# Performance work log

Measured on AMD Instinct MI355X. Metric: run time of the kernel, lower is better.

The kernel has to match this reference:

```python
import jax, jax.numpy as jnp
import numpy as np

B, N, K, C = 4, 4096, 16, 128
BN_EPS = 1e-5


def setup_inputs() -> dict:
    key = jax.random.key(0)
    ks = jax.random.split(key, 16)
    def f(i, shape, s=0.05):
        return jax.random.normal(ks[i], shape, dtype=jnp.float32) * s
    return dict(
        pose_enc=f(0, (B, N, K, 4), 1.0),
        knn_idx=jax.random.randint(ks[1], (B, N, K), 0, N),
        new_points=f(2, (B, N, C), 1.0),
        wq=f(3, (C, C)), wk=f(4, (C, C)), wv=f(5, (C, C)),
        g_w1=f(6, (C, C)), g_b1=jnp.zeros((C,), jnp.float32),
        g_w2=f(7, (C, C)), g_b2=jnp.zeros((C,), jnp.float32),
        d_w1=f(8, (C, 4)), d_b1=jnp.zeros((C,), jnp.float32),
        d_w2=f(9, (C, C)), d_b2=jnp.zeros((C,), jnp.float32),
        c1_w=f(10, (C, C)), c1_b=jnp.zeros((C,), jnp.float32),
        bn1_g=jnp.ones((C,), jnp.float32), bn1_b=jnp.zeros((C,), jnp.float32),
        c2_w=f(11, (C, C)), c2_b=jnp.zeros((C,), jnp.float32),
        bn2_g=jnp.ones((C,), jnp.float32), bn2_b=jnp.zeros((C,), jnp.float32),
    )


def _bn(x, g, b):
    # BatchNorm1d in training mode: stats over (B, N) per channel, biased var
    m = jnp.mean(x, axis=(0, 1))
    v = jnp.mean(jnp.square(x - m), axis=(0, 1))
    return (x - m) * jax.lax.rsqrt(v + BN_EPS) * g + b


def reference(pose_enc, knn_idx, new_points, wq, wk, wv,
              g_w1, g_b1, g_w2, g_b2, d_w1, d_b1, d_w2, d_b2,
              c1_w, c1_b, bn1_g, bn1_b, c2_w, c2_b, bn2_g, bn2_b):
    # fc_delta: (B,N,K,4) -> (B,N,K,C)
    pos = jax.nn.relu(pose_enc @ d_w1.T + d_b1) @ d_w2.T + d_b2
    # CONV2 (1x1 conv == per-point linear) + BN + ReLU on new_points
    x = jax.nn.relu(_bn(new_points @ c2_w.T + c2_b, bn2_g, bn2_b))  # (B,N,C)
    q = x @ wq.T                                   # (B,N,C)
    kf = x @ wk.T
    vf = x @ wv.T
    gather = jax.vmap(lambda pts, idx: pts[idx])   # (B,N,C),(B,N,K)->(B,N,K,C)
    kk = gather(kf, knn_idx)
    vv = gather(vf, knn_idx)
    # fc_gamma vector attention scores
    h = q[:, :, None, :] - kk + pos                # (B,N,K,C)
    attn = jax.nn.relu(h @ g_w1.T + g_b1) @ g_w2.T + g_b2
    # NOTE: original divides by sqrt(k.size(-1)) where k is the key tensor -> sqrt(C)
    attn = jax.nn.softmax(attn / jnp.sqrt(jnp.float32(C)), axis=-2)
    res = jnp.einsum('bmnf,bmnf->bmf', attn, vv + pos)  # (B,N,C)
    res = jax.nn.relu(_bn(res @ c1_w.T + c1_b, bn1_g, bn1_b)) + new_points
    return res
```

## Files before the change

kernel.cpp:

```cpp
#include <hip/hip_runtime.h>
#include <hip/hip_bf16.h>

typedef __bf16 bf16;
typedef __bf16 bf16x4 __attribute__((ext_vector_type(4)));
typedef __bf16 bf16x8 __attribute__((ext_vector_type(8)));
typedef float  f32x4  __attribute__((ext_vector_type(4)));

#define NN 4096
#define KK 16
#define CC 128
#define BN_TOT 16384

__global__ __launch_bounds__(256) void k_lin(
    const float* __restrict__ A, const float* __restrict__ W,
    const float* __restrict__ bias, float* __restrict__ Y,
    float* __restrict__ partial) {
  __shared__ __attribute__((aligned(16))) bf16 WF[32 * 64 * 8];
  __shared__ __attribute__((aligned(16))) float SF[4][16][132];
  __shared__ float P1[128], P2[128];
  int tid = threadIdx.x, w = tid >> 6, l = tid & 63, quad = l >> 4, col = l & 15;
  int r0 = blockIdx.x * 64;
  int arow = r0 + w * 16 + col;

  if (tid < 128) { P1[tid] = 0.f; P2[tid] = 0.f; }

  for (int e = tid; e < 128 * 16; e += 256) {
    int r = e >> 4, c8 = e & 15;
    const float* p = W + r * CC + c8 * 8;
    f32x4 v0 = *(const f32x4*)p, v1 = *(const f32x4*)(p + 4);
    bf16x8 o;
    for (int i = 0; i < 4; i++) { o[i] = (bf16)v0[i]; o[i + 4] = (bf16)v1[i]; }
    int chunk = (r >> 4) * 4 + (c8 >> 2);
    int lane  = (c8 & 3) * 16 + (r & 15);
    *(bf16x8*)(&WF[(chunk * 64 + lane) * 8]) = o;
  }

  bf16x8 a[4];
  for (int kc = 0; kc < 4; kc++) {
    int c0 = kc * 32 + quad * 8;
    f32x4 y0 = *(const f32x4*)(A + arow * CC + c0);
    f32x4 y1 = *(const f32x4*)(A + arow * CC + c0 + 4);
    bf16x8 o;
    for (int i = 0; i < 4; i++) { o[i] = (bf16)y0[i]; o[i + 4] = (bf16)y1[i]; }
    a[kc] = o;
  }

  f32x4 D[8];
  for (int jb = 0; jb < 8; jb++) {
    float bv = bias[jb * 16 + col];
    D[jb] = (f32x4){bv, bv, bv, bv};
  }
  __syncthreads();
  for (int jb = 0; jb < 8; jb++)
    for (int kc = 0; kc < 4; kc++) {
      bf16x8 bfrag = *(const bf16x8*)(&WF[((jb * 4 + kc) * 64 + l) * 8]);
      D[jb] = __builtin_amdgcn_mfma_f32_16x16x32_bf16(a[kc], bfrag, D[jb], 0, 0, 0);
    }

  for (int jb = 0; jb < 8; jb++) {
    float t1 = D[jb][0] + D[jb][1] + D[jb][2] + D[jb][3];
    float t2 = D[jb][0] * D[jb][0] + D[jb][1] * D[jb][1]
             + D[jb][2] * D[jb][2] + D[jb][3] * D[jb][3];
    t1 += __shfl_xor(t1, 16); t1 += __shfl_xor(t1, 32);
    t2 += __shfl_xor(t2, 16); t2 += __shfl_xor(t2, 32);
    if (quad == 0) {
      atomicAdd(&P1[jb * 16 + col], t1);
      atomicAdd(&P2[jb * 16 + col], t2);
    }
  }

  for (int jb = 0; jb < 8; jb++)
    for (int g = 0; g < 4; g++)
      SF[w][quad * 4 + g][jb * 16 + col] = D[jb][g];
  int orow = r0 + w * 16 + (l >> 2), oc0 = (l & 3) * 32;
  for (int c4 = 0; c4 < 8; c4++) {
    f32x4 v = *(const f32x4*)(&SF[w][l >> 2][oc0 + c4 * 4]);
    *(f32x4*)(Y + orow * CC + oc0 + c4 * 4) = v;
  }

  __syncthreads();
  if (tid < 128) {
    partial[blockIdx.x * 256 + tid] = P1[tid];
    partial[blockIdx.x * 256 + 128 + tid] = P2[tid];
  }
}

__global__ __launch_bounds__(1024) void k_finalize(
    const float* __restrict__ partial, const float* __restrict__ g,
    const float* __restrict__ b, float* __restrict__ stats, int NB) {
  __shared__ float sh[2][1024];
  int t = threadIdx.x, c = t & 127, h = t >> 7;
  float s1 = 0.f, s2 = 0.f;
  for (int blk = h; blk < NB; blk += 8) {
    s1 += partial[blk * 256 + c];
    s2 += partial[blk * 256 + 128 + c];
  }
  sh[0][t] = s1; sh[1][t] = s2;
  __syncthreads();
  if (t < 128) {
    s1 = 0.f; s2 = 0.f;
    for (int hh = 0; hh < 8; hh++) {
      s1 += sh[0][hh * 128 + t];
      s2 += sh[1][hh * 128 + t];
    }
    float mean = s1 * (1.0f / BN_TOT);
    float var  = s2 * (1.0f / BN_TOT) - mean * mean;
    float r = rsqrtf(var + 1e-5f);
    float sc = g[t] * r;
    stats[t] = sc;
    stats[128 + t] = b[t] - mean * sc;
  }
}

__global__ __launch_bounds__(256) void k_qkv(
    const float* __restrict__ Y, const float* __restrict__ stats,
    const float* __restrict__ Wq, const float* __restrict__ Wk, const float* __restrict__ Wv,
    bf16* __restrict__ Qo, bf16* __restrict__ Ko, bf16* __restrict__ Vo) {
  __shared__ __attribute__((aligned(16))) bf16 WF[32 * 64 * 8];
  __shared__ __attribute__((aligned(16))) bf16 S[4][16][132];
  int tid = threadIdx.x, w = tid >> 6, l = tid & 63, quad = l >> 4, col = l & 15;
  int j8 = blockIdx.x >> 3, x8 = blockIdx.x & 7;
  int m = j8 >> 5;
  int rb = x8 * 32 + (j8 & 31);
  int r0 = rb * 64;
  int arow = r0 + w * 16 + col;
  const float* Wg = (m == 0) ? Wq : (m == 1) ? Wk : Wv;
  bf16* Os = (m == 0) ? Qo : (m == 1) ? Ko : Vo;

  for (int e = tid; e < 128 * 16; e += 256) {
    int r = e >> 4, c8 = e & 15;
    const float* p = Wg + r * CC + c8 * 8;
    f32x4 v0 = *(const f32x4*)p, v1 = *(const f32x4*)(p + 4);
    bf16x8 o;
    for (int i = 0; i < 4; i++) { o[i] = (bf16)v0[i]; o[i + 4] = (bf16)v1[i]; }
    int chunk = (r >> 4) * 4 + (c8 >> 2);
    int lane  = (c8 & 3) * 16 + (r & 15);
    *(bf16x8*)(&WF[(chunk * 64 + lane) * 8]) = o;
  }

  bf16x8 a[4];
  for (int kc = 0; kc < 4; kc++) {
    int c0 = kc * 32 + quad * 8;
    f32x4 y0  = *(const f32x4*)(Y + arow * CC + c0);
    f32x4 y1  = *(const f32x4*)(Y + arow * CC + c0 + 4);
    f32x4 sc0 = *(const f32x4*)(stats + c0);
    f32x4 sc1 = *(const f32x4*)(stats + c0 + 4);
    f32x4 sf0 = *(const f32x4*)(stats + 128 + c0);
    f32x4 sf1 = *(const f32x4*)(stats + 128 + c0 + 4);
    bf16x8 o;
    for (int i = 0; i < 4; i++) {
      o[i]     = (bf16)fmaxf(y0[i] * sc0[i] + sf0[i], 0.f);
      o[i + 4] = (bf16)fmaxf(y1[i] * sc1[i] + sf1[i], 0.f);
    }
    a[kc] = o;
  }

  __syncthreads();
  f32x4 D[8];
  for (int jb = 0; jb < 8; jb++) D[jb] = (f32x4){0.f, 0.f, 0.f, 0.f};
  for (int jb = 0; jb < 8; jb++)
    for (int kc = 0; kc < 4; kc++) {
      bf16x8 bfrag = *(const bf16x8*)(&WF[((jb * 4 + kc) * 64 + l) * 8]);
      D[jb] = __builtin_amdgcn_mfma_f32_16x16x32_bf16(a[kc], bfrag, D[jb], 0, 0, 0);
    }
  for (int jb = 0; jb < 8; jb++)
    for (int g = 0; g < 4; g++)
      S[w][quad * 4 + g][jb * 16 + col] = (bf16)D[jb][g];
  int orow = r0 + w * 16 + (l >> 2), oc0 = (l & 3) * 32;
  for (int c8 = 0; c8 < 4; c8++) {
    bf16x8 v = *(const bf16x8*)(&S[w][l >> 2][oc0 + c8 * 8]);
    *(bf16x8*)(Os + orow * CC + oc0 + c8 * 8) = v;
  }
}

__global__ __launch_bounds__(256, 1) void k_attn(
    const bf16* __restrict__ Q, const bf16* __restrict__ Kf, const bf16* __restrict__ Vf,
    const int* __restrict__ knn, const float* __restrict__ pose,
    const float* __restrict__ d_w1, const float* __restrict__ d_b1,
    const float* __restrict__ d_w2, const float* __restrict__ d_b2,
    const float* __restrict__ g_w1, const float* __restrict__ g_b1,
    const float* __restrict__ g_w2, const float* __restrict__ g_b2,
    float* __restrict__ Rs) {
  __shared__ __attribute__((aligned(16))) bf16 WF[96 * 64 * 8];
  __shared__ __attribute__((aligned(16))) bf16 S[4][16][132];
  __shared__ __attribute__((aligned(16))) f32x4 DW1v[128];
  __shared__ float DB1[128];

  int tid = threadIdx.x, w = tid >> 6, l = tid & 63, quad = l >> 4, col = l & 15;
  int bid = (blockIdx.x & 7) * 64 + (blockIdx.x >> 3);

  const float* Wg3[3] = {d_w2, g_w1, g_w2};
  for (int m = 0; m < 3; m++) {
    const float* Wg = Wg3[m];
    for (int e = tid; e < 128 * 16; e += 256) {
      int r = e >> 4, c8 = e & 15;
      const float* p = Wg + r * CC + c8 * 8;
      f32x4 v0 = *(const f32x4*)p, v1 = *(const f32x4*)(p + 4);
      bf16x8 o;
      for (int i = 0; i < 4; i++) { o[i] = (bf16)v0[i]; o[i + 4] = (bf16)v1[i]; }
      int chunk = m * 32 + (r >> 4) * 4 + (c8 >> 2);
      int lane  = (c8 & 3) * 16 + (r & 15);
      *(bf16x8*)(&WF[(chunk * 64 + lane) * 8]) = o;
    }
  }
  if (tid < 128) {
    int sc = tid ^ ((tid >> 3) & 7);
    DW1v[sc] = *(const f32x4*)(d_w1 + tid * 4);
    DB1[tid] = d_b1[tid];
  }
  __syncthreads();

  float bR1[8], bR2[8], bR3[8];
#pragma unroll
  for (int jb = 0; jb < 8; jb++) {
    bR1[jb] = d_b2[jb * 16 + col];
    bR2[jb] = g_b1[jb * 16 + col];
    bR3[jb] = g_b2[jb * 16 + col];
  }

  const float smc = 0.08838834764831845f;

#pragma unroll 1
  for (int pp = 0; pp < 4; pp++) {
    int gp0 = bid * 32 + w * 8 + pp * 2;
    int gp1 = gp0 + 1;
    int b   = gp0 >> 12;
    int i0 = knn[gp0 * KK + col];
    int i1 = knn[gp1 * KK + col];
    f32x4 ps0 = *(const f32x4*)(pose + gp0 * 64 + col * 4);
    f32x4 ps1 = *(const f32x4*)(pose + gp1 * 64 + col * 4);

    bf16x8 aA0[4], aA1[4];
#pragma unroll
    for (int kc = 0; kc < 4; kc++) {
      bf16x8 v0, v1;
#pragma unroll
      for (int j = 0; j < 8; j++) {
        int c = kc * 32 + quad * 8 + j;
        f32x4 wr = DW1v[c ^ ((c >> 3) & 7)];
        float db = DB1[c];
        v0[j] = (bf16)fmaxf(ps0[0] * wr[0] + ps0[1] * wr[1] + ps0[2] * wr[2] + ps0[3] * wr[3] + db, 0.f);
        v1[j] = (bf16)fmaxf(ps1[0] * wr[0] + ps1[1] * wr[1] + ps1[2] * wr[2] + ps1[3] * wr[3] + db, 0.f);
      }
      aA0[kc] = v0; aA1[kc] = v1;
    }

    f32x4 D0[8], D1[8];
#pragma unroll
    for (int jb = 0; jb < 8; jb++) {
      float bv = bR1[jb];
      D0[jb] = (f32x4){bv, bv, bv, bv};
      D1[jb] = (f32x4){bv, bv, bv, bv};
    }
#pragma unroll
    for (int jb = 0; jb < 8; jb++)
#pragma unroll
      for (int kc = 0; kc < 4; kc++) {
        bf16x8 bfrag = *(const bf16x8*)(&WF[((jb * 4 + kc) * 64 + l) * 8]);
        D0[jb] = __builtin_amdgcn_mfma_f32_16x16x32_bf16(aA0[kc], bfrag, D0[jb], 0, 0, 0);
        D1[jb] = __builtin_amdgcn_mfma_f32_16x16x32_bf16(aA1[kc], bfrag, D1[jb], 0, 0, 0);
      }

    float vp0[8][4], vp1[8][4];
    {
      int vx0[4], vx1[4];
#pragma unroll
      for (int g = 0; g < 4; g++) {
        vx0[g] = __shfl(i0, quad * 4 + g);
        vx1[g] = __shfl(i1, quad * 4 + g);
      }
#pragma unroll
      for (int g = 0; g < 4; g++) {
        const bf16* vr0 = Vf + ((b << 12) + vx0[g]) * CC + col;
        const bf16* vr1 = Vf + ((b << 12) + vx1[g]) * CC + col;
#pragma unroll
        for (int jb = 0; jb < 8; jb++) {
          vp0[jb][g] = (float)vr0[jb * 16] + D0[jb][g];
          vp1[jb][g] = (float)vr1[jb * 16] + D1[jb][g];
        }
      }
    }

#pragma unroll
    for (int jb = 0; jb < 8; jb++)
#pragma unroll
      for (int g = 0; g < 4; g++)
        S[w][quad * 4 + g][jb * 16 + col] = (bf16)D0[jb][g];
    {
      int grow = (b << 12) + i0;
#pragma unroll
      for (int kc = 0; kc < 4; kc++) {
        int c0 = kc * 32 + quad * 8;
        bf16x8 kkv = *(const bf16x8*)(Kf + grow * CC + c0);
        bf16x8 qv  = *(const bf16x8*)(Q + gp0 * CC + c0);
        bf16x8 pv  = *(const bf16x8*)(&S[w][col][c0]);
        bf16x8 hv;
#pragma unroll
        for (int j = 0; j < 8; j++)
          hv[j] = (bf16)((float)qv[j] - (float)kkv[j] + (float)pv[j]);
        aA0[kc] = hv;
      }
    }
#pragma unroll
    for (int jb = 0; jb < 8; jb++)
#pragma unroll
      for (int g = 0; g < 4; g++)
        S[w][quad * 4 + g][jb * 16 + col] = (bf16)D1[jb][g];
    {
      int grow = (b << 12) + i1;
#pragma unroll
      for (int kc = 0; kc < 4; kc++) {
        int c0 = kc * 32 + quad * 8;
        bf16x8 kkv = *(const bf16x8*)(Kf + grow * CC + c0);
        bf16x8 qv  = *(const bf16x8*)(Q + gp1 * CC + c0);
        bf16x8 pv  = *(const bf16x8*)(&S[w][col][c0]);
        bf16x8 hv;
#pragma unroll
        for (int j = 0; j < 8; j++)
          hv[j] = (bf16)((float)qv[j] - (float)kkv[j] + (float)pv[j]);
        aA1[kc] = hv;
      }
    }

#pragma unroll
    for (int jb = 0; jb < 8; jb++) {
      float bv = bR2[jb];
      D0[jb] = (f32x4){bv, bv, bv, bv};
      D1[jb] = (f32x4){bv, bv, bv, bv};
    }
#pragma unroll
    for (int jb = 0; jb < 8; jb++)
#pragma unroll
      for (int kc = 0; kc < 4; kc++) {
        bf16x8 bfrag = *(const bf16x8*)(&WF[((32 + jb * 4 + kc) * 64 + l) * 8]);
        D0[jb] = __builtin_amdgcn_mfma_f32_16x16x32_bf16(aA0[kc], bfrag, D0[jb], 0, 0, 0);
        D1[jb] = __builtin_amdgcn_mfma_f32_16x16x32_bf16(aA1[kc], bfrag, D1[jb], 0, 0, 0);
      }
#pragma unroll
    for (int jb = 0; jb < 8; jb++)
#pragma unroll
      for (int g = 0; g < 4; g++)
        S[w][quad * 4 + g][jb * 16 + col] = (bf16)fmaxf(D0[jb][g], 0.f);
#pragma unroll
    for (int kc = 0; kc < 4; kc++)
      aA0[kc] = *(const bf16x8*)(&S[w][col][kc * 32 + quad * 8]);
#pragma unroll
    for (int jb = 0; jb < 8; jb++)
#pragma unroll
      for (int g = 0; g < 4; g++)
        S[w][quad * 4 + g][jb * 16 + col] = (bf16)fmaxf(D1[jb][g], 0.f);
#pragma unroll
    for (int kc = 0; kc < 4; kc++)
      aA1[kc] = *(const bf16x8*)(&S[w][col][kc * 32 + quad * 8]);

#pragma unroll
    for (int jb = 0; jb < 8; jb++) {
      float bv = bR3[jb];
      D0[jb] = (f32x4){bv, bv, bv, bv};
      D1[jb] = (f32x4){bv, bv, bv, bv};
    }
#pragma unroll
    for (int jb = 0; jb < 8; jb++)
#pragma unroll
      for (int kc = 0; kc < 4; kc++) {
        bf16x8 bfrag = *(const bf16x8*)(&WF[((64 + jb * 4 + kc) * 64 + l) * 8]);
        D0[jb] = __builtin_amdgcn_mfma_f32_16x16x32_bf16(aA0[kc], bfrag, D0[jb], 0, 0, 0);
        D1[jb] = __builtin_amdgcn_mfma_f32_16x16x32_bf16(aA1[kc], bfrag, D1[jb], 0, 0, 0);
      }

#pragma unroll
    for (int jb = 0; jb < 8; jb++) {
      float s0 = 0.f, pa0 = 0.f, s1 = 0.f, pa1 = 0.f;
#pragma unroll
      for (int g = 0; g < 4; g++) {
        float e0 = __expf(D0[jb][g] * smc);
        float e1 = __expf(D1[jb][g] * smc);
        s0 += e0; pa0 += e0 * vp0[jb][g];
        s1 += e1; pa1 += e1 * vp1[jb][g];
      }
      s0  += __shfl_xor(s0, 16);  s0  += __shfl_xor(s0, 32);
      pa0 += __shfl_xor(pa0, 16); pa0 += __shfl_xor(pa0, 32);
      s1  += __shfl_xor(s1, 16);  s1  += __shfl_xor(s1, 32);
      pa1 += __shfl_xor(pa1, 16); pa1 += __shfl_xor(pa1, 32);
      if (quad == 0) {
        Rs[gp0 * CC + jb * 16 + col] = pa0 / s0;
        Rs[gp1 * CC + jb * 16 + col] = pa1 / s1;
      }
    }
  }
}

__global__ __launch_bounds__(256) void k_out(
    const float* __restrict__ Y, const float* __restrict__ stats,
    const float* __restrict__ NP, float* __restrict__ Out) {
  int i0 = (blockIdx.x * 256 + threadIdx.x) * 4;
  int c0 = i0 & 127;
  f32x4 y  = *(const f32x4*)(Y + i0);
  f32x4 sc = *(const f32x4*)(stats + c0);
  f32x4 sh = *(const f32x4*)(stats + 128 + c0);
  f32x4 np = *(const f32x4*)(NP + i0);
  f32x4 o;
  for (int i = 0; i < 4; i++)
    o[i] = fmaxf(y[i] * sc[i] + sh[i], 0.f) + np[i];
  *(f32x4*)(Out + i0) = o;
}

__global__ void k_code(float* out, float code) {
  if (threadIdx.x == 0) out[1000003] = code;
}

extern "C" void kernel_launch(void* const* d_in, const int* in_sizes, int n_in,
                              void* d_out, int out_size, void* d_ws, size_t ws_size,
                              hipStream_t stream) {
  static const int expect[22] = {
    1048576, 262144, 2097152, 16384, 16384, 16384,
    16384, 128, 16384, 128,
    512, 128, 16384, 128,
    16384, 128, 128, 128,
    16384, 128, 128, 128
  };
  if (n_in != 22) { k_code<<<1, 64, 0, stream>>>((float*)d_out, 4194304.f); return; }
  for (int i = 0; i < 22; i++)
    if (in_sizes[i] != expect[i]) {
      k_code<<<1, 64, 0, stream>>>((float*)d_out, 262144.f * (float)(i + 1));
      return;
    }

  const float* pose  = (const float*)d_in[0];
  const int*   knn   = (const int*)d_in[1];
  const float* np_   = (const float*)d_in[2];
  const float* wq    = (const float*)d_in[3];
  const float* wk    = (const float*)d_in[4];
  const float* wv    = (const float*)d_in[5];
  const float* g_w1  = (const float*)d_in[6];
  const float* g_b1  = (const float*)d_in[7];
  const float* g_w2  = (const float*)d_in[8];
  const float* g_b2  = (const float*)d_in[9];
  const float* d_w1  = (const float*)d_in[10];
  const float* d_b1  = (const float*)d_in[11];
  const float* d_w2  = (const float*)d_in[12];
  const float* d_b2  = (const float*)d_in[13];
  const float* c1_w  = (const float*)d_in[14];
  const float* c1_b  = (const float*)d_in[15];
  const float* bn1_g = (const float*)d_in[16];
  const float* bn1_b = (const float*)d_in[17];
  const float* c2_w  = (const float*)d_in[18];
  const float* c2_b  = (const float*)d_in[19];
  const float* bn2_g = (const float*)d_in[20];
  const float* bn2_b = (const float*)d_in[21];

  float* y2      = (float*)d_ws;
  float* res     = y2 + 2097152;
  bf16*  qf      = (bf16*)(res + 2097152);
  bf16*  kf      = qf + 2097152;
  bf16*  vf      = kf + 2097152;
  float* partial = (float*)(vf + 2097152);
  float* stats2  = partial + 65536;
  float* stats1  = stats2 + 256;

  size_t NEED = (size_t)((char*)(stats1 + 256) - (char*)d_ws);
  if (ws_size < NEED) {
    k_code<<<1, 64, 0, stream>>>((float*)d_out, 2097152.f);
    return;
  }

  k_lin     <<<256, 256, 0, stream>>>(np_, c2_w, c2_b, y2, partial);
  k_finalize<<<1, 1024, 0, stream>>>(partial, bn2_g, bn2_b, stats2, 256);
  k_qkv     <<<768, 256, 0, stream>>>(y2, stats2, wq, wk, wv, qf, kf, vf);
  k_attn    <<<512, 256, 0, stream>>>(qf, kf, vf, knn, pose,
                                      d_w1, d_b1, d_w2, d_b2,
                                      g_w1, g_b1, g_w2, g_b2, res);
  k_lin     <<<256, 256, 0, stream>>>(res, c1_w, c1_b, y2, partial);
  k_finalize<<<1, 1024, 0, stream>>>(partial, bn1_g, bn1_b, stats1, 256);
  k_out     <<<2048, 256, 0, stream>>>(y2, stats1, np_, (float*)d_out);
}
```

Baseline: 240.1 us.

## Shrink attention kernel LDS to allow two blocks per CU

Removes the d_w2 fragment, d_w1 and d_b1 tables from shared memory. d_w2 fragments are now loaded straight from global memory and converted to bf16 on the fly, and d_w1/d_b1 are read from global. The staging buffer gets an XOR-swizzled layout to cut bank conflicts. The launch bound is raised to two blocks per CU so a second block can hide latency, at the cost of a tighter register budget and repeated global/L2 loads plus conversions of d_w2 in every iteration.

Measured after the change: 363.2 us. +51.3%, slower.

```diff
diff --git a/kernel.cpp b/kernel.cpp
--- a/kernel.cpp
+++ b/kernel.cpp
@@ -173,7 +173,7 @@
   }
 }
 
-__global__ __launch_bounds__(256, 1) void k_attn(
+__global__ __launch_bounds__(256, 2) void k_attn(
     const bf16* __restrict__ Q, const bf16* __restrict__ Kf, const bf16* __restrict__ Vf,
     const int* __restrict__ knn, const float* __restrict__ pose,
     const float* __restrict__ d_w1, const float* __restrict__ d_b1,
@@ -181,17 +181,15 @@
     const float* __restrict__ g_w1, const float* __restrict__ g_b1,
     const float* __restrict__ g_w2, const float* __restrict__ g_b2,
     float* __restrict__ Rs) {
-  __shared__ __attribute__((aligned(16))) bf16 WF[96 * 64 * 8];
-  __shared__ __attribute__((aligned(16))) bf16 S[4][16][132];
-  __shared__ __attribute__((aligned(16))) f32x4 DW1v[128];
-  __shared__ float DB1[128];
+  __shared__ __attribute__((aligned(16))) bf16 WF[64 * 64 * 8];
+  __shared__ __attribute__((aligned(16))) bf16 S[4][2048];
 
   int tid = threadIdx.x, w = tid >> 6, l = tid & 63, quad = l >> 4, col = l & 15;
   int bid = (blockIdx.x & 7) * 64 + (blockIdx.x >> 3);
 
-  const float* Wg3[3] = {d_w2, g_w1, g_w2};
-  for (int m = 0; m < 3; m++) {
-    const float* Wg = Wg3[m];
+  const float* Wg2[2] = {g_w1, g_w2};
+  for (int m = 0; m < 2; m++) {
+    const float* Wg = Wg2[m];
     for (int e = tid; e < 128 * 16; e += 256) {
       int r = e >> 4, c8 = e & 15;
       const float* p = Wg + r * CC + c8 * 8;
@@ -203,11 +201,6 @@
       *(bf16x8*)(&WF[(chunk * 64 + lane) * 8]) = o;
     }
   }
-  if (tid < 128) {
-    int sc = tid ^ ((tid >> 3) & 7);
-    DW1v[sc] = *(const f32x4*)(d_w1 + tid * 4);
-    DB1[tid] = d_b1[tid];
-  }
   __syncthreads();
 
   float bR1[8], bR2[8], bR3[8];
@@ -218,7 +211,17 @@
     bR3[jb] = g_b2[jb * 16 + col];
   }
 
+  char* Sw = (char*)&S[w][0];
   const float smc = 0.08838834764831845f;
+
+  auto ldfragW = [&](const float* __restrict__ Wp, int jb, int kc) -> bf16x8 {
+    const float* p = Wp + (jb * 16 + col) * CC + kc * 32 + quad * 8;
+    f32x4 v0 = *(const f32x4*)p, v1 = *(const f32x4*)(p + 4);
+    bf16x8 o;
+#pragma unroll
+    for (int i = 0; i < 4; i++) { o[i] = (bf16)v0[i]; o[i + 4] = (bf16)v1[i]; }
+    return o;
+  };
 
 #pragma unroll 1
   for (int pp = 0; pp < 4; pp++) {
@@ -237,8 +240,8 @@
 #pragma unroll
       for (int j = 0; j < 8; j++) {
         int c = kc * 32 + quad * 8 + j;
-        f32x4 wr = DW1v[c ^ ((c >> 3) & 7)];
-        float db = DB1[c];
+        f32x4 wr = *(const f32x4*)(d_w1 + c * 4);
+        float db = d_b1[c];
         v0[j] = (bf16)fmaxf(ps0[0] * wr[0] + ps0[1] * wr[1] + ps0[2] * wr[2] + ps0[3] * wr[3] + db, 0.f);
         v1[j] = (bf16)fmaxf(ps1[0] * wr[0] + ps1[1] * wr[1] + ps1[2] * wr[2] + ps1[3] * wr[3] + db, 0.f);
       }
@@ -252,6 +255,93 @@
       D0[jb] = (f32x4){bv, bv, bv, bv};
       D1[jb] = (f32x4){bv, bv, bv, bv};
     }
+#pragma unroll 2
+    for (int jb = 0; jb < 8; jb++) {
+      bf16x8 bf0 = ldfragW(d_w2, jb, 0);
+      bf16x8 bf1 = ldfragW(d_w2, jb, 1);
+      bf16x8 bf2 = ldfragW(d_w2, jb, 2);
+      bf16x8 bf3 = ldfragW(d_w2, jb, 3);
+      D0[jb] = __builtin_amdgcn_mfma_f32_16x16x32_bf16(aA0[0], bf0, D0[jb], 0, 0, 0);
+      D1[jb] = __builtin_amdgcn_mfma_f32_16x16x32_bf16(aA1[0], bf0, D1[jb], 0, 0, 0);
+      D0[jb] = __builtin_amdgcn_mfma_f32_16x16x32_bf16(aA0[1], bf1, D0[jb], 0, 0, 0);
+      D1[jb] = __builtin_amdgcn_mfma_f32_16x16x32_bf16(aA1[1], bf1, D1[jb], 0, 0, 0);
+      D0[jb] = __builtin_amdgcn_mfma_f32_16x16x32_bf16(aA0[2], bf2, D0[jb], 0, 0, 0);
+      D1[jb] = __builtin_amdgcn_mfma_f32_16x16x32_bf16(aA1[2], bf2, D1[jb], 0, 0, 0);
+      D0[jb] = __builtin_amdgcn_mfma_f32_16x16x32_bf16(aA0[3], bf3, D0[jb], 0, 0, 0);
+      D1[jb] = __builtin_amdgcn_mfma_f32_16x16x32_bf16(aA1[3], bf3, D1[jb], 0, 0, 0);
+    }
+
+    float vp0[8][4], vp1[8][4];
+    {
+      int vx0[4], vx1[4];
+#pragma unroll
+      for (int g = 0; g < 4; g++) {
+        vx0[g] = __shfl(i0, quad * 4 + g);
+        vx1[g] = __shfl(i1, quad * 4 + g);
+      }
+#pragma unroll
+      for (int g = 0; g < 4; g++) {
+        const bf16* vr0 = Vf + ((b << 12) + vx0[g]) * CC + col;
+        const bf16* vr1 = Vf + ((b << 12) + vx1[g]) * CC + col;
+#pragma unroll
+        for (int jb = 0; jb < 8; jb++) {
+          vp0[jb][g] = (float)vr0[jb * 16] + D0[jb][g];
+          vp1[jb][g] = (float)vr1[jb * 16] + D1[jb][g];
+        }
+      }
+    }
+
+#pragma unroll
+    for (int jb = 0; jb < 8; jb++)
+#pragma unroll
+      for (int g = 0; g < 4; g++) {
+        int r = quad * 4 + g;
+        *(bf16*)(Sw + r * 256 + (((jb * 16 + col) * 2) ^ ((r & 7) << 4))) = (bf16)D0[jb][g];
+      }
+    {
+      int grow = (b << 12) + i0;
+#pragma unroll
+      for (int kc = 0; kc < 4; kc++) {
+        int c0 = kc * 32 + quad * 8;
+        bf16x8 kkv = *(const bf16x8*)(Kf + grow * CC + c0);
+        bf16x8 qv  = *(const bf16x8*)(Q + gp0 * CC + c0);
+        bf16x8 pv  = *(const bf16x8*)(Sw + col * 256 + ((kc * 64 + quad * 16) ^ ((col & 7) << 4)));
+        bf16x8 hv;
+#pragma unroll
+        for (int j = 0; j < 8; j++)
+          hv[j] = (bf16)((float)qv[j] - (float)kkv[j] + (float)pv[j]);
+        aA0[kc] = hv;
+      }
+    }
+#pragma unroll
+    for (int jb = 0; jb < 8; jb++)
+#pragma unroll
+      for (int g = 0; g < 4; g++) {
+        int r = quad * 4 + g;
+        *(bf16*)(Sw + r * 256 + (((jb * 16 + col) * 2) ^ ((r & 7) << 4))) = (bf16)D1[jb][g];
+      }
+    {
+      int grow = (b << 12) + i1;
+#pragma unroll
+      for (int kc = 0; kc < 4; kc++) {
+        int c0 = kc * 32 + quad * 8;
+        bf16x8 kkv = *(const bf16x8*)(Kf + grow * CC + c0);
+        bf16x8 qv  = *(const bf16x8*)(Q + gp1 * CC + c0);
+        bf16x8 pv  = *(const bf16x8*)(Sw + col * 256 + ((kc * 64 + quad * 16) ^ ((col & 7) << 4)));
+        bf16x8 hv;
+#pragma unroll
+        for (int j = 0; j < 8; j++)
+          hv[j] = (bf16)((float)qv[j] - (float)kkv[j] + (float)pv[j]);
+        aA1[kc] = hv;
+      }
+    }
+
+#pragma unroll
+    for (int jb = 0; jb < 8; jb++) {
+      float bv = bR2[jb];
+      D0[jb] = (f32x4){bv, bv, bv, bv};
+      D1[jb] = (f32x4){bv, bv, bv, bv};
+    }
 #pragma unroll
     for (int jb = 0; jb < 8; jb++)
 #pragma unroll
@@ -260,98 +350,26 @@
         D0[jb] = __builtin_amdgcn_mfma_f32_16x16x32_bf16(aA0[kc], bfrag, D0[jb], 0, 0, 0);
         D1[jb] = __builtin_amdgcn_mfma_f32_16x16x32_bf16(aA1[kc], bfrag, D1[jb], 0, 0, 0);
       }
-
-    float vp0[8][4], vp1[8][4];
-    {
-      int vx0[4], vx1[4];
-#pragma unroll
-      for (int g = 0; g < 4; g++) {
-        vx0[g] = __shfl(i0, quad * 4 + g);
-        vx1[g] = __shfl(i1, quad * 4 + g);
-      }
-#pragma unroll
-      for (int g = 0; g < 4; g++) {
-        const bf16* vr0 = Vf + ((b << 12) + vx0[g]) * CC + col;
-        const bf16* vr1 = Vf + ((b << 12) + vx1[g]) * CC + col;
-#pragma unroll
-        for (int jb = 0; jb < 8; jb++) {
-          vp0[jb][g] = (float)vr0[jb * 16] + D0[jb][g];
-          vp1[jb][g] = (float)vr1[jb * 16] + D1[jb][g];
-        }
-      }
-    }
-
-#pragma unroll
-    for (int jb = 0; jb < 8; jb++)
-#pragma unroll
-      for (int g = 0; g < 4; g++)
-        S[w][quad * 4 + g][jb * 16 + col] = (bf16)D0[jb][g];
-    {
-      int grow = (b << 12) + i0;
-#pragma unroll
-      for (int kc = 0; kc < 4; kc++) {
-        int c0 = kc * 32 + quad * 8;
-        bf16x8 kkv = *(const bf16x8*)(Kf + grow * CC + c0);
-        bf16x8 qv  = *(const bf16x8*)(Q + gp0 * CC + c0);
-        bf16x8 pv  = *(const bf16x8*)(&S[w][col][c0]);
-        bf16x8 hv;
-#pragma unroll
-        for (int j = 0; j < 8; j++)
-          hv[j] = (bf16)((float)qv[j] - (float)kkv[j] + (float)pv[j]);
-        aA0[kc] = hv;
-      }
-    }
-#pragma unroll
-    for (int jb = 0; jb < 8; jb++)
-#pragma unroll
-      for (int g = 0; g < 4; g++)
-        S[w][quad * 4 + g][jb * 16 + col] = (bf16)D1[jb][g];
-    {
-      int grow = (b << 12) + i1;
-#pragma unroll
-      for (int kc = 0; kc < 4; kc++) {
-        int c0 = kc * 32 + quad * 8;
-        bf16x8 kkv = *(const bf16x8*)(Kf + grow * CC + c0);
-        bf16x8 qv  = *(const bf16x8*)(Q + gp1 * CC + c0);
-        bf16x8 pv  = *(const bf16x8*)(&S[w][col][c0]);
-        bf16x8 hv;
-#pragma unroll
-        for (int j = 0; j < 8; j++)
-          hv[j] = (bf16)((float)qv[j] - (float)kkv[j] + (float)pv[j]);
-        aA1[kc] = hv;
-      }
-    }
-
-#pragma unroll
-    for (int jb = 0; jb < 8; jb++) {
-      float bv = bR2[jb];
-      D0[jb] = (f32x4){bv, bv, bv, bv};
-      D1[jb] = (f32x4){bv, bv, bv, bv};
-    }
-#pragma unroll
-    for (int jb = 0; jb < 8; jb++)
-#pragma unroll
-      for (int kc = 0; kc < 4; kc++) {
-        bf16x8 bfrag = *(const bf16x8*)(&WF[((32 + jb * 4 + kc) * 64 + l) * 8]);
-        D0[jb] = __builtin_amdgcn_mfma_f32_16x16x32_bf16(aA0[kc], bfrag, D0[jb], 0, 0, 0);
-        D1[jb] = __builtin_amdgcn_mfma_f32_16x16x32_bf16(aA1[kc], bfrag, D1[jb], 0, 0, 0);
-      }
-#pragma unroll
-    for (int jb = 0; jb < 8; jb++)
-#pragma unroll
-      for (int g = 0; g < 4; g++)
-        S[w][quad * 4 + g][jb * 16 + col] = (bf16)fmaxf(D0[jb][g], 0.f);
+#pragma unroll
+    for (int jb = 0; jb < 8; jb++)
+#pragma unroll
+      for (int g = 0; g < 4; g++) {
+        int r = quad * 4 + g;
+        *(bf16*)(Sw + r * 256 + (((jb * 16 + col) * 2) ^ ((r & 7) << 4))) = (bf16)fmaxf(D0[jb][g], 0.f);
+      }
 #pragma unroll
     for (int kc = 0; kc < 4; kc++)
-      aA0[kc] = *(const bf16x8*)(&S[w][col][kc * 32 + quad * 8]);
-#pragma unroll
-    for (int jb = 0; jb < 8; jb++)
-#pragma unroll
-      for (int g = 0; g < 4; g++)
-        S[w][quad * 4 + g][jb * 16 + col] = (bf16)fmaxf(D1[jb][g], 0.f);
+      aA0[kc] = *(const bf16x8*)(Sw + col * 256 + ((kc * 64 + quad * 16) ^ ((col & 7) << 4)));
+#pragma unroll
+    for (int jb = 0; jb < 8; jb++)
+#pragma unroll
+      for (int g = 0; g < 4; g++) {
+        int r = quad * 4 + g;
+        *(bf16*)(Sw + r * 256 + (((jb * 16 + col) * 2) ^ ((r & 7) << 4))) = (bf16)fmaxf(D1[jb][g], 0.f);
+      }
 #pragma unroll
     for (int kc = 0; kc < 4; kc++)
-      aA1[kc] = *(const bf16x8*)(&S[w][col][kc * 32 + quad * 8]);
+      aA1[kc] = *(const bf16x8*)(Sw + col * 256 + ((kc * 64 + quad * 16) ^ ((col & 7) << 4)));
 
 #pragma unroll
     for (int jb = 0; jb < 8; jb++) {
@@ -363,7 +381,7 @@
     for (int jb = 0; jb < 8; jb++)
 #pragma unroll
       for (int kc = 0; kc < 4; kc++) {
-        bf16x8 bfrag = *(const bf16x8*)(&WF[((64 + jb * 4 + kc) * 64 + l) * 8]);
+        bf16x8 bfrag = *(const bf16x8*)(&WF[((32 + jb * 4 + kc) * 64 + l) * 8]);
         D0[jb] = __builtin_amdgcn_mfma_f32_16x16x32_bf16(aA0[kc], bfrag, D0[jb], 0, 0, 0);
         D1[jb] = __builtin_amdgcn_mfma_f32_16x16x32_bf16(aA1[kc], bfrag, D1[jb], 0, 0, 0);
       }
```
